# Performance work log

Hardware: AMD Instinct MI355X
Metric: run time of the kernel (lower is better)

## Reference

```python
import jax, jax.numpy as jnp
import numpy as np
import math

D = 512; H = 8; L = 6; FF = 2048; S = 512; B = 32; IN = 64; OUT = 1
HD = D // H
EPS = 1e-5


def _pos_encoding(seq_len, d_model):
    position = jnp.arange(seq_len, dtype=jnp.float32)[:, None]
    div_term = jnp.exp(jnp.arange(0, d_model, 2, dtype=jnp.float32) * (-math.log(10000.0) / d_model))
    ang = position * div_term  # [S, D/2]
    pe = jnp.zeros((seq_len, d_model), dtype=jnp.float32)
    pe = pe.at[:, 0::2].set(jnp.sin(ang)).at[:, 1::2].set(jnp.cos(ang))
    return pe


def _layernorm(x, g, b):
    m = jnp.mean(x, axis=-1, keepdims=True)
    v = jnp.mean((x - m) ** 2, axis=-1, keepdims=True)
    return (x - m) * jax.lax.rsqrt(v + EPS) * g + b


def setup_inputs() -> dict:
    key = jax.random.key(0)
    ks = jax.random.split(key, 20)
    s = 0.02
    return {
        "src": jax.random.normal(ks[0], (B, S, IN), dtype=jnp.float32),
        "inp_w": jax.random.uniform(ks[1], (D, IN), minval=-0.1, maxval=0.1, dtype=jnp.float32),
        "inp_b": jnp.zeros((D,), dtype=jnp.float32),
        "in_proj_w": jax.random.normal(ks[2], (L, 3 * D, D), dtype=jnp.float32) * s,
        "in_proj_b": jnp.zeros((L, 3 * D), dtype=jnp.float32),
        "out_w": jax.random.normal(ks[3], (L, D, D), dtype=jnp.float32) * s,
        "out_b": jnp.zeros((L, D), dtype=jnp.float32),
        "ff_w1": jax.random.normal(ks[4], (L, FF, D), dtype=jnp.float32) * s,
        "ff_b1": jnp.zeros((L, FF), dtype=jnp.float32),
        "ff_w2": jax.random.normal(ks[5], (L, D, FF), dtype=jnp.float32) * s,
        "ff_b2": jnp.zeros((L, D), dtype=jnp.float32),
        "ln1_g": jnp.ones((L, D), dtype=jnp.float32),
        "ln1_b": jnp.zeros((L, D), dtype=jnp.float32),
        "ln2_g": jnp.ones((L, D), dtype=jnp.float32),
        "ln2_b": jnp.zeros((L, D), dtype=jnp.float32),
        "op_w1": jax.random.normal(ks[6], (FF, D), dtype=jnp.float32) * s,
        "op_b1": jnp.zeros((FF,), dtype=jnp.float32),
        "op_w2": jax.random.normal(ks[7], (OUT, FF), dtype=jnp.float32) * s,
        "op_b2": jnp.zeros((OUT,), dtype=jnp.float32),
    }


def reference(src, inp_w, inp_b, in_proj_w, in_proj_b, out_w, out_b,
              ff_w1, ff_b1, ff_w2, ff_b2, ln1_g, ln1_b, ln2_g, ln2_b,
              op_w1, op_b1, op_w2, op_b2):
    # input projection + sqrt(d_model) scale + positional encoding
    x = (src @ inp_w.T + inp_b) * math.sqrt(D)
    x = x + _pos_encoding(S, D)[None, :, :]
    scale = 1.0 / math.sqrt(HD)
    for i in range(L):
        # self-attention (torch nn.MultiheadAttention, eval mode, no mask)
        qkv = x @ in_proj_w[i].T + in_proj_b[i]            # [B,S,3D]
        q, k, v = jnp.split(qkv, 3, axis=-1)
        q = q.reshape(B, S, H, HD).transpose(0, 2, 1, 3)   # [B,H,S,HD]
        k = k.reshape(B, S, H, HD).transpose(0, 2, 1, 3)
        v = v.reshape(B, S, H, HD).transpose(0, 2, 1, 3)
        scores = jnp.einsum('bhqd,bhkd->bhqk', q, k) * scale
        attn = jax.nn.softmax(scores, axis=-1)             # [B,H,S,S]
        o = jnp.einsum('bhqk,bhkd->bhqd', attn, v)
        o = o.transpose(0, 2, 1, 3).reshape(B, S, D)
        o = o @ out_w[i].T + out_b[i]
        x = _layernorm(x + o, ln1_g[i], ln1_b[i])
        # feedforward
        h = jax.nn.relu(x @ ff_w1[i].T + ff_b1[i])
        ff = h @ ff_w2[i].T + ff_b2[i]
        x = _layernorm(x + ff, ln2_g[i], ln2_b[i])
    # take last timestep, output projection MLP
    last = x[:, -1, :]                                     # [B,D]
    h = jax.nn.relu(last @ op_w1.T + op_b1)
    return h @ op_w2.T + op_b2                             # [B,OUT]
```

## Files before the change

### kernel.cpp

```cpp
#include <hip/hip_runtime.h>

typedef short s16x8 __attribute__((ext_vector_type(8)));
typedef float f32x4 __attribute__((ext_vector_type(4)));
typedef float f32x16 __attribute__((ext_vector_type(16)));

__device__ short g_wbuf[18874368];
__device__ short g_srcb[1048576];
__device__ short g_inpwb[32768];
__device__ float g_pe[262144];
__device__ float g_hpart[256];

__device__ inline float b2f(short s) {
  union { unsigned int u; float f; } v;
  v.u = ((unsigned int)(unsigned short)s) << 16;
  return v.f;
}
__device__ inline short f2b(float f) {
  union { float f; unsigned int u; } v; v.f = f;
  unsigned int r = (v.u + 0x7fffu + ((v.u >> 16) & 1u)) >> 16;
  return (short)r;
}
__device__ inline s16x8 pack8(float4 a, float4 b) {
  s16x8 r;
  r[0] = f2b(a.x); r[1] = f2b(a.y); r[2] = f2b(a.z); r[3] = f2b(a.w);
  r[4] = f2b(b.x); r[5] = f2b(b.y); r[6] = f2b(b.z); r[7] = f2b(b.w);
  return r;
}

__device__ inline f32x4 mfma16(s16x8 a, s16x8 b, f32x4 c) {
  return __builtin_amdgcn_mfma_f32_16x16x32_bf16(a, b, c, 0, 0, 0);
}
__device__ inline f32x16 mfma32(s16x8 a, s16x8 b, f32x16 c) {
  return __builtin_amdgcn_mfma_f32_32x32x16_bf16(a, b, c, 0, 0, 0);
}

typedef const __attribute__((address_space(1))) void* as1cptr;
typedef __attribute__((address_space(3))) void* as3ptr;
__device__ inline void gl2lds16(const short* g, short* l) {
  __builtin_amdgcn_global_load_lds((as1cptr)g, (as3ptr)l, 16, 0, 0);
}

__global__ void __launch_bounds__(256)
cvt2_kernel(const float* __restrict__ i0, const float* __restrict__ i1) {
  const int b = blockIdx.x;
  const float* src; short* dst; int base;
  if (b < 512) { src = i0; dst = g_srcb; base = b; }
  else         { src = i1; dst = g_inpwb; base = b - 512; }
  const int idx = (base * 256 + threadIdx.x) * 8;
  float4 a = *(const float4*)(src + idx);
  float4 c = *(const float4*)(src + idx + 4);
  *(s16x8*)(dst + idx) = pack8(a, c);
}

__global__ void __launch_bounds__(256)
cvt6_kernel(const float* __restrict__ i0, const float* __restrict__ i1,
            const float* __restrict__ i2, const float* __restrict__ i3) {
  const int b = blockIdx.x;
  const float* src; short* dst; int base;
  if (b < 2304)      { src = i0; dst = g_wbuf;            base = b; }
  else if (b < 3072) { src = i1; dst = g_wbuf +  4718592; base = b - 2304; }
  else if (b < 6144) { src = i2; dst = g_wbuf +  6291456; base = b - 3072; }
  else               { src = i3; dst = g_wbuf + 12582912; base = b - 6144; }
  const int idx = (base * 256 + threadIdx.x) * 8;
  float4 a = *(const float4*)(src + idx);
  float4 c = *(const float4*)(src + idx + 4);
  *(s16x8*)(dst + idx) = pack8(a, c);
}

__global__ void __launch_bounds__(256)
pe_kernel() {
  const int s = blockIdx.x;
  const int n0 = threadIdx.x * 2;
  const float ang = (float)s * expf((float)n0 * -0.0179889460390160f);
  g_pe[s * 512 + n0]     = sinf(ang);
  g_pe[s * 512 + n0 + 1] = cosf(ang);
}

template <int EPI>
__global__ void __launch_bounds__(256, 3)
gemm_bt(const short* __restrict__ Ain, int woff, const float* __restrict__ bias,
        short* __restrict__ C, int M, int N, int K) {
  __shared__ short As[128 * 64];
  __shared__ short Bs[128 * 64];
  const int tid  = threadIdx.x;
  const int lane = tid & 63;
  const int wave = tid >> 6;
  const int wr = (wave >> 1) << 6;
  const int wc = (wave & 1) << 6;
  const int l31 = lane & 31;
  const int half = lane >> 5;
  const int bm = blockIdx.x & 127;
  const int bn = blockIdx.x >> 7;

  const short* A = (EPI == 2) ? (const short*)g_srcb : Ain;
  const short* W = (EPI == 2) ? (const short*)g_inpwb : (const short*)(g_wbuf + woff);

  int srow[4], soff[4];
#pragma unroll
  for (int i = 0; i < 4; ++i) {
    const int u = i * 256 + tid;
    srow[i] = u >> 3;
    soff[i] = ((u & 7) ^ ((u >> 3) & 7)) << 3;
  }
  const int rsw = lane & 7;
  f32x16 acc[2][2] = {};

  for (int k0 = 0; k0 < K; k0 += 64) {
#pragma unroll
    for (int i = 0; i < 4; ++i) {
      gl2lds16(A + (size_t)(bm * 128 + srow[i]) * K + k0 + soff[i],
               As + (i * 256 + tid) * 8);
      gl2lds16(W + (size_t)(bn * 128 + srow[i]) * K + k0 + soff[i],
               Bs + (i * 256 + tid) * 8);
    }
    __syncthreads();
#pragma unroll
    for (int ks = 0; ks < 4; ++ks) {
      const int rchunk = ((ks * 2 + half) ^ rsw) * 8;
      s16x8 af[2], bfr[2];
#pragma unroll
      for (int i = 0; i < 2; ++i)
        af[i] = *(const s16x8*)(As + (wr + i * 32 + l31) * 64 + rchunk);
#pragma unroll
      for (int j = 0; j < 2; ++j)
        bfr[j] = *(const s16x8*)(Bs + (wc + j * 32 + l31) * 64 + rchunk);
#pragma unroll
      for (int i = 0; i < 2; ++i)
#pragma unroll
        for (int j = 0; j < 2; ++j)
          acc[i][j] = mfma32(af[i], bfr[j], acc[i][j]);
    }
    __syncthreads();
  }

#pragma unroll
  for (int j = 0; j < 2; ++j) {
    const int col = bn * 128 + wc + j * 32 + l31;
    const float bv = bias[col];
#pragma unroll
    for (int i = 0; i < 2; ++i) {
      const int rbase = bm * 128 + wr + i * 32 + half * 4;
#pragma unroll
      for (int r = 0; r < 16; ++r) {
        const int row = rbase + (r & 3) + 8 * (r >> 2);
        float v = acc[i][j][r] + bv;
        if (EPI == 1) v = fmaxf(v, 0.0f);
        if (EPI == 2) {
          const int s = row & 511;
          v = (acc[i][j][r] + bv) * 22.62741699796952f + g_pe[s * 512 + col];
        }
        C[(size_t)row * N + col] = f2b(v);
      }
    }
  }
}

__global__ void __launch_bounds__(512, 4)
attn_kernel(const short* __restrict__ qkv, short* __restrict__ ctx) {
  __shared__ short Kb[8192];
  __shared__ short VT[8192];
  __shared__ short Pt[8192];
  __shared__ float rcomb[2][4][16];
  const int tid = threadIdx.x;
  const int lane = tid & 63, wave = tid >> 6;
  const int ml = lane & 15, quad = lane >> 4;
  const int mt = wave >> 1, nh = wave & 1;
  const int qt = (blockIdx.x >> 3) & 7;
  const int bh = (blockIdx.x & 7) | ((blockIdx.x >> 6) << 3);
  const int b = bh >> 3, h = bh & 7;
  const size_t basebs = (size_t)b * 512 * 1536;
  const int hoff = h * 64;

  s16x8 qf0, qf1;
  {
    const int qrow = qt * 64 + mt * 16 + ml;
    const short* qp = qkv + basebs + (size_t)qrow * 1536 + hoff;
    qf0 = *(const s16x8*)(qp + quad * 8);
    qf1 = *(const s16x8*)(qp + 32 + quad * 8);
  }

  const int srow0 = tid >> 3, srow1 = srow0 + 64;
  const int soff0 = (((tid & 7) ^ (srow0 & 7)) << 3);
  const int soff1 = (((tid & 7) ^ (srow1 & 7)) << 3);
  const short* kbase = qkv + basebs + 512 + hoff;

  const int vkp = tid & 63, vd8 = (tid >> 6) << 3;
  const short* vbase = qkv + basebs + 1024 + hoff + vd8;

  gl2lds16(kbase + (size_t)srow0 * 1536 + soff0, &Kb[tid * 8]);
  gl2lds16(kbase + (size_t)srow1 * 1536 + soff1, &Kb[(512 + tid) * 8]);
  __syncthreads();

  f32x4 oacc[2] = {};
  float psum[4] = {0.f, 0.f, 0.f, 0.f};
  float mrun[4] = {-1e30f, -1e30f, -1e30f, -1e30f};

#pragma unroll 1
  for (int rr = 0; rr < 4; ++rr) {
    const short* vp = vbase + (size_t)(rr * 128 + vkp * 2) * 1536;
    s16x8 va = *(const s16x8*)vp;
    s16x8 vb = *(const s16x8*)(vp + 1536);

    f32x4 sc[4];
#pragma unroll
    for (int nt = 0; nt < 4; ++nt) {
      const int krow = nh * 64 + nt * 16 + ml;
      const short* kr = Kb + krow * 64;
      s16x8 kf0 = *(const s16x8*)(kr + ((quad ^ (ml & 7)) << 3));
      s16x8 kf1 = *(const s16x8*)(kr + (((quad + 4) ^ (ml & 7)) << 3));
      f32x4 s0 = {};
      s0 = mfma16(qf0, kf0, s0);
      s0 = mfma16(qf1, kf1, s0);
      sc[nt] = s0;
    }

#pragma unroll
    for (int j = 0; j < 8; ++j) {
      const int d = vd8 + j;
      unsigned int u = (unsigned int)(unsigned short)va[j]
                     | ((unsigned int)(unsigned short)vb[j] << 16);
      *(unsigned int*)(VT + d * 128 + ((((vkp >> 2) ^ (d & 15)) << 3) | ((vkp & 3) << 1))) = u;
    }

    f32x4 tmx = sc[0];
#pragma unroll
    for (int nt = 1; nt < 4; ++nt)
#pragma unroll
      for (int r = 0; r < 4; ++r)
        tmx[r] = fmaxf(tmx[r], sc[nt][r]);
#pragma unroll
    for (int off = 1; off <= 8; off <<= 1)
#pragma unroll
      for (int r = 0; r < 4; ++r)
        tmx[r] = fmaxf(tmx[r], __shfl_xor(tmx[r], off));
    if (ml == 0) {
#pragma unroll
      for (int r = 0; r < 4; ++r)
        rcomb[nh][mt][quad * 4 + r] = tmx[r];
    }
    __syncthreads();

    if (rr < 3) {
      const short* kb2 = kbase + (size_t)((rr + 1) * 128) * 1536;
      gl2lds16(kb2 + (size_t)srow0 * 1536 + soff0, &Kb[tid * 8]);
      gl2lds16(kb2 + (size_t)srow1 * 1536 + soff1, &Kb[(512 + tid) * 8]);
    }

#pragma unroll
    for (int r = 0; r < 4; ++r) {
      const float tm = 0.125f * fmaxf(rcomb[0][mt][quad * 4 + r],
                                      rcomb[1][mt][quad * 4 + r]);
      const float mn = fmaxf(mrun[r], tm);
      const float scl = __expf(mrun[r] - mn);
      mrun[r] = mn;
      psum[r] *= scl;
      oacc[0][r] *= scl;
      oacc[1][r] *= scl;
    }

#pragma unroll
    for (int nt = 0; nt < 4; ++nt) {
#pragma unroll
      for (int r = 0; r < 4; ++r) {
        union { float f; unsigned int u; } pu;
        pu.f = __expf(sc[nt][r] * 0.125f - mrun[r]);
        const short pb = (short)(pu.u >> 16);
        pu.u &= 0xffff0000u;
        psum[r] += pu.f;
        const int qrl = mt * 16 + quad * 4 + r;
        const int c = nh * 64 + nt * 16 + ml;
        Pt[qrl * 128 + ((((c >> 3) ^ (qrl & 15)) << 3) | (c & 7))] = pb;
      }
    }
    __syncthreads();

    const int prow = mt * 16 + ml;
#pragma unroll
    for (int ks = 0; ks < 4; ++ks) {
      s16x8 pf = *(const s16x8*)(Pt + prow * 128 + ((((ks << 2) | quad) ^ ml) << 3));
#pragma unroll
      for (int n2 = 0; n2 < 2; ++n2) {
        const int nd = (nh * 2 + n2) * 16 + ml;
        s16x8 vf = *(const s16x8*)(VT + nd * 128 + ((((ks << 2) | quad) ^ ml) << 3));
        oacc[n2] = mfma16(pf, vf, oacc[n2]);
      }
    }
    __syncthreads();
  }

#pragma unroll
  for (int off = 1; off <= 8; off <<= 1)
#pragma unroll
    for (int r = 0; r < 4; ++r)
      psum[r] += __shfl_xor(psum[r], off);
  if (ml == 0) {
#pragma unroll
    for (int r = 0; r < 4; ++r)
      rcomb[nh][mt][quad * 4 + r] = psum[r];
  }
  __syncthreads();

#pragma unroll
  for (int r = 0; r < 4; ++r) {
    const float l = rcomb[0][mt][quad * 4 + r] + rcomb[1][mt][quad * 4 + r];
    const float rl = 1.0f / l;
    const int grow = qt * 64 + mt * 16 + quad * 4 + r;
#pragma unroll
    for (int n2 = 0; n2 < 2; ++n2) {
      const int d = (nh * 2 + n2) * 16 + ml;
      ctx[((size_t)b * 512 + grow) * 512 + hoff + d] = f2b(oacc[n2][r] * rl);
    }
  }
}

__global__ void __launch_bounds__(256)
ln_kernel(short* __restrict__ x, const short* __restrict__ o,
          const float* __restrict__ g, const float* __restrict__ bta) {
  const int row = blockIdx.x * 4 + (threadIdx.x >> 6);
  const int lane = threadIdx.x & 63;
  short* xp = x + (size_t)row * 512 + lane * 8;
  const short* op = o + (size_t)row * 512 + lane * 8;
  s16x8 xv = *(const s16x8*)xp;
  s16x8 ov = *(const s16x8*)op;
  float v[8]; float s = 0.f, s2 = 0.f;
#pragma unroll
  for (int e = 0; e < 8; ++e) {
    float f = b2f(xv[e]) + b2f(ov[e]);
    v[e] = f; s += f; s2 += f * f;
  }
#pragma unroll
  for (int off = 32; off >= 1; off >>= 1) {
    s += __shfl_xor(s, off);
    s2 += __shfl_xor(s2, off);
  }
  const float mean = s * (1.f / 512.f);
  const float var = s2 * (1.f / 512.f) - mean * mean;
  const float rstd = rsqrtf(var + 1e-5f);
  float4 g0 = *(const float4*)(g + lane * 8);
  float4 g1 = *(const float4*)(g + lane * 8 + 4);
  float4 b0 = *(const float4*)(bta + lane * 8);
  float4 b1 = *(const float4*)(bta + lane * 8 + 4);
  float gv[8] = {g0.x, g0.y, g0.z, g0.w, g1.x, g1.y, g1.z, g1.w};
  float bv[8] = {b0.x, b0.y, b0.z, b0.w, b1.x, b1.y, b1.z, b1.w};
  s16x8 outv;
#pragma unroll
  for (int e = 0; e < 8; ++e)
    outv[e] = f2b((v[e] - mean) * rstd * gv[e] + bv[e]);
  *(s16x8*)xp = outv;
}

__global__ void __launch_bounds__(256)
head1_kernel(const short* __restrict__ x, const float* __restrict__ w1,
             const float* __restrict__ b1, const float* __restrict__ w2) {
  const int bidx = blockIdx.x;
  const int b = bidx >> 3, seg = bidx & 7;
  const int tid = threadIdx.x;
  __shared__ float xl[512];
  __shared__ float red[256];
  for (int n = tid; n < 512; n += 256)
    xl[n] = b2f(x[((size_t)b * 512 + 511) * 512 + n]);
  __syncthreads();
  const int f = seg * 256 + tid;
  const float* wr = w1 + (size_t)f * 512;
  float hv = 0.f;
  for (int k8 = 0; k8 < 64; ++k8) {
    float4 wa = *(const float4*)(wr + k8 * 8);
    float4 wb = *(const float4*)(wr + k8 * 8 + 4);
    hv += xl[k8 * 8 + 0] * wa.x + xl[k8 * 8 + 1] * wa.y +
          xl[k8 * 8 + 2] * wa.z + xl[k8 * 8 + 3] * wa.w +
          xl[k8 * 8 + 4] * wb.x + xl[k8 * 8 + 5] * wb.y +
          xl[k8 * 8 + 6] * wb.z + xl[k8 * 8 + 7] * wb.w;
  }
  hv += b1[f];
  hv = fmaxf(hv, 0.f);
  red[tid] = hv * w2[f];
  __syncthreads();
  for (int stride = 128; stride > 0; stride >>= 1) {
    if (tid < stride) red[tid] += red[tid + stride];
    __syncthreads();
  }
  if (tid == 0) g_hpart[bidx] = red[0];
}

__global__ void __launch_bounds__(64)
head2_kernel(const float* __restrict__ b2, float* __restrict__ out) {
  const int t = threadIdx.x;
  if (t < 32) {
    float s = 0.f;
#pragma unroll
    for (int c = 0; c < 8; ++c) s += g_hpart[t * 8 + c];
    out[t] = s + b2[0];
  }
}

extern "C" void kernel_launch(void* const* d_in, const int* in_sizes, int n_in,
                              void* d_out, int out_size, void* d_ws, size_t ws_size,
                              hipStream_t stream) {
  (void)in_sizes; (void)n_in; (void)out_size; (void)ws_size;
  const float* src       = (const float*)d_in[0];
  const float* inp_w     = (const float*)d_in[1];
  const float* inp_b     = (const float*)d_in[2];
  const float* in_proj_w = (const float*)d_in[3];
  const float* in_proj_b = (const float*)d_in[4];
  const float* out_w     = (const float*)d_in[5];
  const float* out_b     = (const float*)d_in[6];
  const float* ff_w1     = (const float*)d_in[7];
  const float* ff_b1     = (const float*)d_in[8];
  const float* ff_w2     = (const float*)d_in[9];
  const float* ff_b2     = (const float*)d_in[10];
  const float* ln1_g     = (const float*)d_in[11];
  const float* ln1_b     = (const float*)d_in[12];
  const float* ln2_g     = (const float*)d_in[13];
  const float* ln2_b     = (const float*)d_in[14];
  const float* op_w1     = (const float*)d_in[15];
  const float* op_b1     = (const float*)d_in[16];
  const float* op_w2     = (const float*)d_in[17];
  const float* op_b2     = (const float*)d_in[18];

  short* ws   = (short*)d_ws;
  short* x    = ws;
  short* qkv  = ws + 8388608;
  short* ctx  = qkv + 25165824;
  short* obuf = ctx + 8388608;
  short* h    = qkv;

  cvt2_kernel<<<528, 256, 0, stream>>>(src, inp_w);
  cvt6_kernel<<<9216, 256, 0, stream>>>(in_proj_w, out_w, ff_w1, ff_w2);
  pe_kernel<<<512, 256, 0, stream>>>();
  gemm_bt<2><<<512, 256, 0, stream>>>(nullptr, 0, inp_b, x, 16384, 512, 64);

  for (int l = 0; l < 6; ++l) {
    const int w_qkv = l * 786432;
    const int w_out = 4718592 + l * 262144;
    const int w_ff1 = 6291456 + l * 1048576;
    const int w_ff2 = 12582912 + l * 1048576;
    gemm_bt<0><<<1536, 256, 0, stream>>>(
        x, w_qkv, in_proj_b + l * 1536, qkv, 16384, 1536, 512);
    attn_kernel<<<2048, 512, 0, stream>>>(qkv, ctx);
    gemm_bt<0><<<512, 256, 0, stream>>>(
        ctx, w_out, out_b + l * 512, obuf, 16384, 512, 512);
    ln_kernel<<<4096, 256, 0, stream>>>(x, obuf, ln1_g + l * 512, ln1_b + l * 512);
    gemm_bt<1><<<2048, 256, 0, stream>>>(
        x, w_ff1, ff_b1 + l * 2048, h, 16384, 2048, 512);
    gemm_bt<0><<<512, 256, 0, stream>>>(
        h, w_ff2, ff_b2 + l * 512, obuf, 16384, 512, 2048);
    ln_kernel<<<4096, 256, 0, stream>>>(x, obuf, ln2_g + l * 512, ln2_b + l * 512);
  }
  head1_kernel<<<256, 256, 0, stream>>>(x, op_w1, op_b1, op_w2);
  head2_kernel<<<1, 64, 0, stream>>>(op_b2, (float*)d_out);
}
```

Baseline: 1.543 ms.

## Software-pipeline attention PV step, use exp2 softmax, and group GEMM block order

```diff
diff --git a/kernel.cpp b/kernel.cpp
--- a/kernel.cpp
+++ b/kernel.cpp
@@ -89,8 +89,12 @@
   const int wc = (wave & 1) << 6;
   const int l31 = lane & 31;
   const int half = lane >> 5;
-  const int bm = blockIdx.x & 127;
-  const int bn = blockIdx.x >> 7;
+  const int bnc = N >> 7;
+  const int per = bnc << 5;
+  const int g   = blockIdx.x / per;
+  const int rix = blockIdx.x - g * per;
+  const int bm  = (g << 5) + (rix & 31);
+  const int bn  = rix >> 5;
 
   const short* A = (EPI == 2) ? (const short*)g_srcb : Ain;
   const short* W = (EPI == 2) ? (const short*)g_inpwb : (const short*)(g_wbuf + woff);
@@ -170,6 +174,7 @@
   const int b = bh >> 3, h = bh & 7;
   const size_t basebs = (size_t)b * 512 * 1536;
   const int hoff = h * 64;
+  const float C2 = 0.18033688011112042f;
 
   s16x8 qf0, qf1;
   {
@@ -194,14 +199,23 @@
   f32x4 oacc[2] = {};
   float psum[4] = {0.f, 0.f, 0.f, 0.f};
   float mrun[4] = {-1e30f, -1e30f, -1e30f, -1e30f};
+  const int prow = mt * 16 + ml;
+  f32x4 sc[4];
 
 #pragma unroll 1
   for (int rr = 0; rr < 4; ++rr) {
-    const short* vp = vbase + (size_t)(rr * 128 + vkp * 2) * 1536;
-    s16x8 va = *(const s16x8*)vp;
-    s16x8 vb = *(const s16x8*)(vp + 1536);
-
-    f32x4 sc[4];
+    if (rr > 0) {
+#pragma unroll
+      for (int ks = 0; ks < 4; ++ks) {
+        s16x8 pf = *(const s16x8*)(Pt + prow * 128 + ((((ks << 2) | quad) ^ ml) << 3));
+#pragma unroll
+        for (int n2 = 0; n2 < 2; ++n2) {
+          const int nd = (nh * 2 + n2) * 16 + ml;
+          s16x8 vf = *(const s16x8*)(VT + nd * 128 + ((((ks << 2) | quad) ^ ml) << 3));
+          oacc[n2] = mfma16(pf, vf, oacc[n2]);
+        }
+      }
+    }
 #pragma unroll
     for (int nt = 0; nt < 4; ++nt) {
       const int krow = nh * 64 + nt * 16 + ml;
@@ -213,15 +227,6 @@
       s0 = mfma16(qf1, kf1, s0);
       sc[nt] = s0;
     }
-
-#pragma unroll
-    for (int j = 0; j < 8; ++j) {
-      const int d = vd8 + j;
-      unsigned int u = (unsigned int)(unsigned short)va[j]
-                     | ((unsigned int)(unsigned short)vb[j] << 16);
-      *(unsigned int*)(VT + d * 128 + ((((vkp >> 2) ^ (d & 15)) << 3) | ((vkp & 3) << 1))) = u;
-    }
-
     f32x4 tmx = sc[0];
 #pragma unroll
     for (int nt = 1; nt < 4; ++nt)
@@ -240,30 +245,31 @@
     }
     __syncthreads();
 
+    const short* vp = vbase + (size_t)(rr * 128 + vkp * 2) * 1536;
+    s16x8 va = *(const s16x8*)vp;
+    s16x8 vb = *(const s16x8*)(vp + 1536);
     if (rr < 3) {
       const short* kb2 = kbase + (size_t)((rr + 1) * 128) * 1536;
       gl2lds16(kb2 + (size_t)srow0 * 1536 + soff0, &Kb[tid * 8]);
       gl2lds16(kb2 + (size_t)srow1 * 1536 + soff1, &Kb[(512 + tid) * 8]);
     }
-
 #pragma unroll
     for (int r = 0; r < 4; ++r) {
-      const float tm = 0.125f * fmaxf(rcomb[0][mt][quad * 4 + r],
-                                      rcomb[1][mt][quad * 4 + r]);
+      const float tm = C2 * fmaxf(rcomb[0][mt][quad * 4 + r],
+                                  rcomb[1][mt][quad * 4 + r]);
       const float mn = fmaxf(mrun[r], tm);
-      const float scl = __expf(mrun[r] - mn);
+      const float scl = exp2f(mrun[r] - mn);
       mrun[r] = mn;
       psum[r] *= scl;
       oacc[0][r] *= scl;
       oacc[1][r] *= scl;
     }
-
 #pragma unroll
     for (int nt = 0; nt < 4; ++nt) {
 #pragma unroll
       for (int r = 0; r < 4; ++r) {
         union { float f; unsigned int u; } pu;
-        pu.f = __expf(sc[nt][r] * 0.125f - mrun[r]);
+        pu.f = exp2f(fmaf(sc[nt][r], C2, -mrun[r]));
         const short pb = (short)(pu.u >> 16);
         pu.u &= 0xffff0000u;
         psum[r] += pu.f;
@@ -272,20 +278,32 @@
         Pt[qrl * 128 + ((((c >> 3) ^ (qrl & 15)) << 3) | (c & 7))] = pb;
       }
     }
+    {
+      const unsigned int* vau = (const unsigned int*)&va;
+      const unsigned int* vbu = (const unsigned int*)&vb;
+#pragma unroll
+      for (int k = 0; k < 4; ++k) {
+        const int d0 = vd8 + 2 * k;
+        unsigned int lo = __builtin_amdgcn_perm(vbu[k], vau[k], 0x05040100u);
+        unsigned int hi = __builtin_amdgcn_perm(vbu[k], vau[k], 0x07060302u);
+        *(unsigned int*)(VT + d0 * 128 +
+            ((((vkp >> 2) ^ (d0 & 15)) << 3) | ((vkp & 3) << 1))) = lo;
+        *(unsigned int*)(VT + (d0 + 1) * 128 +
+            ((((vkp >> 2) ^ ((d0 + 1) & 15)) << 3) | ((vkp & 3) << 1))) = hi;
+      }
+    }
     __syncthreads();
-
-    const int prow = mt * 16 + ml;
-#pragma unroll
-    for (int ks = 0; ks < 4; ++ks) {
-      s16x8 pf = *(const s16x8*)(Pt + prow * 128 + ((((ks << 2) | quad) ^ ml) << 3));
-#pragma unroll
-      for (int n2 = 0; n2 < 2; ++n2) {
-        const int nd = (nh * 2 + n2) * 16 + ml;
-        s16x8 vf = *(const s16x8*)(VT + nd * 128 + ((((ks << 2) | quad) ^ ml) << 3));
-        oacc[n2] = mfma16(pf, vf, oacc[n2]);
-      }
-    }
-    __syncthreads();
+  }
+
+#pragma unroll
+  for (int ks = 0; ks < 4; ++ks) {
+    s16x8 pf = *(const s16x8*)(Pt + prow * 128 + ((((ks << 2) | quad) ^ ml) << 3));
+#pragma unroll
+    for (int n2 = 0; n2 < 2; ++n2) {
+      const int nd = (nh * 2 + n2) * 16 + ml;
+      s16x8 vf = *(const s16x8*)(VT + nd * 128 + ((((ks << 2) | quad) ^ ml) << 3));
+      oacc[n2] = mfma16(pf, vf, oacc[n2]);
+    }
   }
 
 #pragma unroll
```

After: 1.493 ms. 3.2% less time.
